# Performance work log

Measured on AMD Instinct MI355X. Metric: run time of the kernel, lower is better.

## Reference

```python
import jax, jax.numpy as jnp
import numpy as np
import math

B = 64        # graphs per batch
NPG = 2048    # nodes per graph
DEG = 4       # avg degree
EPG = NPG * DEG
N = B * NPG
E = B * EPG
F_IN = 4
H = 128
K1 = math.ceil(0.8 * NPG)   # 1639
K2 = math.ceil(0.8 * K1)    # 1312
K3 = math.ceil(0.8 * K2)    # 1050
ACT = 124


def setup_inputs() -> dict:
    key = jax.random.key(0)
    ks = jax.random.split(key, 20)
    x = jax.random.normal(ks[0], (N, F_IN), jnp.float32)
    off = (jnp.arange(B, dtype=jnp.int32) * NPG)[:, None]
    src = (jax.random.randint(ks[1], (B, EPG), 0, NPG, jnp.int32) + off).reshape(-1)
    dst = (jax.random.randint(ks[2], (B, EPG), 0, NPG, jnp.int32) + off).reshape(-1)

    def lin(k, fi, fo):
        return (jax.random.normal(k, (fi, fo), jnp.float32) / np.sqrt(fi)).astype(jnp.float32)

    return dict(
        x=x, src=src, dst=dst,
        W1=lin(ks[3], F_IN, H), b1=jnp.zeros((H,), jnp.float32),
        W2=lin(ks[4], H, H),    b2=jnp.zeros((H,), jnp.float32),
        W3=lin(ks[5], H, H),    b3=jnp.zeros((H,), jnp.float32),
        p1=jax.random.normal(ks[6], (H,), jnp.float32),
        p2=jax.random.normal(ks[7], (H,), jnp.float32),
        p3=jax.random.normal(ks[8], (H,), jnp.float32),
        lw1=lin(ks[9], 2 * H, H),  lb1=jnp.zeros((H,), jnp.float32),
        lw2=lin(ks[10], H, 64),    lb2=jnp.zeros((64,), jnp.float32),
        lw3=lin(ks[11], 64, ACT),  lb3=jnp.zeros((ACT,), jnp.float32),
    )


def gcn(x, W, b, src, dst, emask, n_nodes):
    # PyG GCNConv: add self loops, sym-norm deg^-1/2 A deg^-1/2, then bias
    h = x @ W                                  # [n, H]
    w = emask.astype(x.dtype)                  # [E]
    deg = jax.ops.segment_sum(w, dst, num_segments=n_nodes) + 1.0  # +1 self loop
    dis = jax.lax.rsqrt(deg)
    coef = dis[src] * dis[dst] * w             # [E]
    out = jax.ops.segment_sum(h[src] * coef[:, None], dst, num_segments=n_nodes)
    out = out + h * (dis * dis)[:, None]       # self-loop contribution
    return out + b


def topk_pool(x, p, src, dst, emask, n_per_graph, k):
    # TopKPooling: score = tanh(x.p/||p||); keep top ceil(ratio*n) per graph;
    # x_out = x[perm] * score[perm]; drop edges not fully inside kept set.
    score = jnp.tanh((x @ p) / jnp.linalg.norm(p))       # [B*n]
    vals, idx = jax.lax.top_k(score.reshape(B, n_per_graph), k)  # [B,k]
    xg = x.reshape(B, n_per_graph, -1)
    x_new = (jnp.take_along_axis(xg, idx[:, :, None], axis=1) * vals[:, :, None])
    x_new = x_new.reshape(B * k, -1)
    flat_idx = (idx + (jnp.arange(B, dtype=jnp.int32) * n_per_graph)[:, None]).reshape(-1)
    new_pos = jnp.full((B * n_per_graph,), -1, jnp.int32)
    new_pos = new_pos.at[flat_idx].set(jnp.arange(B * k, dtype=jnp.int32))
    ns, nd = new_pos[src], new_pos[dst]
    valid = emask & (ns >= 0) & (nd >= 0)
    ns = jnp.where(valid, ns, 0)
    nd = jnp.where(valid, nd, 0)
    return x_new, ns, nd, valid


def readout(x, k):
    # global_max_pool || global_mean_pool (uniform graph sizes)
    xr = x.reshape(B, k, -1)
    return jnp.concatenate([xr.max(axis=1), xr.mean(axis=1)], axis=1)  # [B, 2H]


def reference(x, src, dst, W1, b1, W2, b2, W3, b3, p1, p2, p3,
              lw1, lb1, lw2, lb2, lw3, lb3):
    emask = jnp.ones((E,), bool)
    h = jax.nn.relu(gcn(x, W1, b1, src, dst, emask, N))
    h, s1, d1, m1 = topk_pool(h, p1, src, dst, emask, NPG, K1)
    x1 = readout(h, K1)
    h = jax.nn.relu(gcn(h, W2, b2, s1, d1, m1, B * K1))
    h, s2, d2, m2 = topk_pool(h, p2, s1, d1, m1, K1, K2)
    x2 = readout(h, K2)
    h = jax.nn.relu(gcn(h, W3, b3, s2, d2, m2, B * K2))
    h, s3, d3, m3 = topk_pool(h, p3, s2, d2, m2, K2, K3)
    x3 = readout(h, K3)
    z = x1 + x2 + x3                                # [B, 256]
    z = jax.nn.relu(z @ lw1 + lb1)
    z = jax.nn.relu(z @ lw2 + lb2)
    # F.dropout(p=0.5) is identity in eval mode
    out = jax.nn.sigmoid(z @ lw3 + lb3)             # [B, 124]; squeeze(1) is no-op
    return out
```

## Files before the change

kernel.cpp:

```cpp
#include <hip/hip_runtime.h>
#include <math.h>

namespace {
constexpr int B_   = 64;
constexpr int NPG  = 2048;
constexpr int N0   = B_ * NPG;
constexpr int E0   = N0 * 4;
constexpr int H_   = 128;
constexpr int K1   = 1639, K2 = 1312, K3 = 1050;
constexpr int N1   = B_ * K1;
constexpr int N2   = B_ * K2;
constexpr int N3   = B_ * K3;
constexpr int ACT  = 124;
constexpr int RS   = 32;
}

__global__ __launch_bounds__(256) void mmh_k(const float* __restrict__ Xin,
                                             const int* __restrict__ selOld,
                                             const float* __restrict__ score,
                                             const float* __restrict__ W,
                                             float* __restrict__ C, int M)
{
    __shared__ float sA[64 * 128];
    int tid = threadIdx.x;
    int row0 = blockIdx.x * 64;
    #pragma unroll
    for (int ch = 0; ch < 8; ++ch) {
        int i = ch * 1024 + tid * 4;
        int r = i >> 7, c = i & 127;
        int g = selOld[row0 + r];
        float sc = score[g];
        float4 v = *(const float4*)(Xin + (size_t)g * H_ + c);
        v.x *= sc; v.y *= sc; v.z *= sc; v.w *= sc;
        *(float4*)(sA + i) = v;
    }
    __syncthreads();
    int c4 = (tid & 31) * 4;
    int rg = tid >> 5;
    const float* sArow = sA + rg * 8 * 128;
    float4 acc[8];
    #pragma unroll
    for (int q = 0; q < 8; ++q) acc[q] = make_float4(0.f, 0.f, 0.f, 0.f);

    const float* Wp = W + c4;
    float4 w0 = *(const float4*)(Wp + 0 * 128);
    float4 w1 = *(const float4*)(Wp + 1 * 128);
    float4 w2 = *(const float4*)(Wp + 2 * 128);
    float4 w3 = *(const float4*)(Wp + 3 * 128);
    #pragma unroll 1
    for (int g4 = 0; g4 < 31; ++g4) {
        int kk = g4 * 4;
        const float* Wn = Wp + (kk + 4) * 128;
        float4 n0 = *(const float4*)(Wn + 0 * 128);
        float4 n1 = *(const float4*)(Wn + 1 * 128);
        float4 n2 = *(const float4*)(Wn + 2 * 128);
        float4 n3 = *(const float4*)(Wn + 3 * 128);
        #pragma unroll
        for (int q = 0; q < 8; ++q) {
            float4 a = *(const float4*)(sArow + q * 128 + kk);
            acc[q].x += a.x * w0.x; acc[q].y += a.x * w0.y; acc[q].z += a.x * w0.z; acc[q].w += a.x * w0.w;
            acc[q].x += a.y * w1.x; acc[q].y += a.y * w1.y; acc[q].z += a.y * w1.z; acc[q].w += a.y * w1.w;
            acc[q].x += a.z * w2.x; acc[q].y += a.z * w2.y; acc[q].z += a.z * w2.z; acc[q].w += a.z * w2.w;
            acc[q].x += a.w * w3.x; acc[q].y += a.w * w3.y; acc[q].z += a.w * w3.z; acc[q].w += a.w * w3.w;
        }
        w0 = n0; w1 = n1; w2 = n2; w3 = n3;
    }
    {
        const int kk = 124;
        #pragma unroll
        for (int q = 0; q < 8; ++q) {
            float4 a = *(const float4*)(sArow + q * 128 + kk);
            acc[q].x += a.x * w0.x; acc[q].y += a.x * w0.y; acc[q].z += a.x * w0.z; acc[q].w += a.x * w0.w;
            acc[q].x += a.y * w1.x; acc[q].y += a.y * w1.y; acc[q].z += a.y * w1.z; acc[q].w += a.y * w1.w;
            acc[q].x += a.z * w2.x; acc[q].y += a.z * w2.y; acc[q].z += a.z * w2.z; acc[q].w += a.z * w2.w;
            acc[q].x += a.w * w3.x; acc[q].y += a.w * w3.y; acc[q].z += a.w * w3.z; acc[q].w += a.w * w3.w;
        }
    }
    #pragma unroll
    for (int q = 0; q < 8; ++q) {
        int r = row0 + rg * 8 + q;
        *(float4*)(C + (size_t)r * H_ + c4) = acc[q];
    }
}

__global__ void count_deg_k(const int* __restrict__ dst, int E, int* __restrict__ deg)
{
    int e = blockIdx.x * blockDim.x + threadIdx.x;
    if (e < E) atomicAdd(deg + dst[e], 1);
}

__global__ __launch_bounds__(1024) void scan1_k(const int* __restrict__ in, int* __restrict__ out,
                                                int* __restrict__ bsum, int n)
{
    __shared__ int s[1024];
    int t = threadIdx.x;
    int i = blockIdx.x * 1024 + t;
    int v = (i < n) ? in[i] : 0;
    s[t] = v;
    __syncthreads();
    for (int d = 1; d < 1024; d <<= 1) {
        int add = (t >= d) ? s[t - d] : 0;
        __syncthreads();
        s[t] += add;
        __syncthreads();
    }
    if (i < n) out[i] = s[t] - v;
    if (t == 1023) bsum[blockIdx.x] = s[1023];
}

__global__ __launch_bounds__(256) void scan2_k(int* __restrict__ bsum, int nb,
                                               int* __restrict__ totalOut,
                                               const float* __restrict__ p,
                                               float* __restrict__ invnOut)
{
    __shared__ int s[256];
    __shared__ float ps[128];
    int t = threadIdx.x;
    int v = (t < nb) ? bsum[t] : 0;
    s[t] = v;
    if (p && t < 128) ps[t] = p[t] * p[t];
    __syncthreads();
    for (int d = 1; d < 256; d <<= 1) {
        int add = (t >= d) ? s[t - d] : 0;
        __syncthreads();
        s[t] += add;
        __syncthreads();
    }
    if (t < nb) bsum[t] = s[t] - v;
    if (t == 0 && totalOut) *totalOut = s[255];
    for (int d = 64; d > 0; d >>= 1) {
        if (p && t < d) ps[t] += ps[t + d];
        __syncthreads();
    }
    if (p && t == 0) *invnOut = rsqrtf(ps[0]);
}

__global__ void scan3_k(int* __restrict__ out, const int* __restrict__ bsum, int n,
                        const int* __restrict__ deg, float* __restrict__ dis)
{
    int i = blockIdx.x * blockDim.x + threadIdx.x;
    if (i < n) {
        out[i] += bsum[i >> 10];
        dis[i] = rsqrtf((float)deg[i] + 1.0f);
    }
}

__global__ void fill_k(const int* __restrict__ src, const int* __restrict__ dst, int E,
                       const int* __restrict__ rowoff, int* __restrict__ cur,
                       int* __restrict__ esrc)
{
    int e = blockIdx.x * blockDim.x + threadIdx.x;
    if (e >= E) return;
    int d = dst[e];
    int pos = rowoff[d] + atomicAdd(cur + d, 1);
    esrc[pos] = src[e];
}

__global__ void remap_count_k(const int* __restrict__ osrc, const int* __restrict__ odst,
                              const int* __restrict__ ecntIn, int fixedE,
                              const int* __restrict__ newpos, int* __restrict__ deg)
{
    int E = ecntIn ? *ecntIn : fixedE;
    int e = blockIdx.x * blockDim.x + threadIdx.x;
    if (e >= E) return;
    int ns = newpos[osrc[e]];
    int nd = newpos[odst[e]];
    if (ns >= 0 && nd >= 0) atomicAdd(deg + nd, 1);
}

__global__ void remap_fill_k(const int* __restrict__ osrc, const int* __restrict__ odst,
                             const int* __restrict__ ecntIn, int fixedE,
                             const int* __restrict__ newpos, const int* __restrict__ rowoff,
                             int* __restrict__ cur,
                             int* __restrict__ esrc, int* __restrict__ edst)
{
    int E = ecntIn ? *ecntIn : fixedE;
    int e = blockIdx.x * blockDim.x + threadIdx.x;
    if (e >= E) return;
    int ns = newpos[osrc[e]];
    int nd = newpos[odst[e]];
    if (ns >= 0 && nd >= 0) {
        int pos = rowoff[nd] + atomicAdd(cur + nd, 1);
        esrc[pos] = ns;
        edst[pos] = nd;
    }
}

__global__ __launch_bounds__(256) void aggx_k(const float* __restrict__ X,
                                              const int* __restrict__ rowoff,
                                              const int* __restrict__ esrc,
                                              const float* __restrict__ dis,
                                              const float* __restrict__ W1,
                                              const float* __restrict__ b1,
                                              const float* __restrict__ p1,
                                              const float* __restrict__ invn,
                                              float* __restrict__ out,
                                              float* __restrict__ score,
                                              int npg, int Gb)
{
    __shared__ float sW[512];
    __shared__ float sb[128];
    __shared__ float sp[128];
    __shared__ float sxa[256 * 4];
    __shared__ float sdt[256];
    int tid = threadIdx.x;
    for (int i = tid; i < 512; i += 256) sW[i] = W1[i];
    if (tid < 128) { sb[tid] = b1[tid]; sp[tid] = p1[tid]; }
    int pb = blockIdx.x;
    int x8 = pb & 7;
    int m  = pb >> 3;
    int g  = x8 + 8 * (m / Gb);
    int lb = m % Gb;
    int nbase = g * npg + lb * 256;
    int n = nbase + tid;
    float dn = dis[n];
    float4 xa = *(const float4*)(X + (size_t)n * 4);
    float s2 = dn * dn;
    xa.x *= s2; xa.y *= s2; xa.z *= s2; xa.w *= s2;
    int beg = rowoff[n], end = rowoff[n + 1];
    for (int e = beg; e < end; ++e) {
        int s = esrc[e];
        float c = dis[s] * dn;
        float4 xs = *(const float4*)(X + (size_t)s * 4);
        xa.x += xs.x * c; xa.y += xs.y * c; xa.z += xs.z * c; xa.w += xs.w * c;
    }
    *(float4*)(sxa + tid * 4) = xa;
    __syncthreads();
    int wv = tid >> 6;
    int lane = tid & 63;
    int c0 = lane * 2;
    float wa0 = sW[c0],     wb0 = sW[128 + c0],     wc0 = sW[256 + c0],     wd0 = sW[384 + c0];
    float wa1 = sW[c0 + 1], wb1 = sW[128 + c0 + 1], wc1 = sW[256 + c0 + 1], wd1 = sW[384 + c0 + 1];
    float bb0 = sb[c0], bb1 = sb[c0 + 1];
    float pp0 = sp[c0], pp1 = sp[c0 + 1];
    #pragma unroll 4
    for (int ii = 0; ii < 64; ++ii) {
        int i = wv * 64 + ii;
        float4 a = *(const float4*)(sxa + i * 4);
        float o0 = fmaxf(a.x * wa0 + a.y * wb0 + a.z * wc0 + a.w * wd0 + bb0, 0.f);
        float o1 = fmaxf(a.x * wa1 + a.y * wb1 + a.z * wc1 + a.w * wd1 + bb1, 0.f);
        ((float2*)(out + (size_t)(nbase + i) * H_))[lane] = make_float2(o0, o1);
        float dt = o0 * pp0 + o1 * pp1;
        for (int mm = 32; mm > 0; mm >>= 1) dt += __shfl_xor(dt, mm);
        if (lane == 0) sdt[i] = dt;
    }
    __syncthreads();
    score[nbase + tid] = tanhf(sdt[tid] * invn[0]);
}

__global__ __launch_bounds__(256) void agg_k(const float* __restrict__ Hf,
                                             const int* __restrict__ rowoff,
                                             const int* __restrict__ esrc,
                                             const float* __restrict__ dis,
                                             const float* __restrict__ bias,
                                             const float* __restrict__ p,
                                             const float* __restrict__ invn,
                                             float* __restrict__ out,
                                             float* __restrict__ score,
                                             int npg, int Gb)
{
    int pb = blockIdx.x;
    int x8 = pb & 7;
    int m  = pb >> 3;
    int g  = x8 + 8 * (m / Gb);
    int lb = m % Gb;
    int j  = lb * 4 + (threadIdx.x >> 6);
    if (j >= npg) return;
    int n = g * npg + j;
    int lane = threadIdx.x & 63;
    int half = lane >> 5;
    int l4 = (lane & 31) * 4;
    float dn = dis[n];
    int beg = rowoff[n], end = rowoff[n + 1];
    float4 acc = make_float4(0.f, 0.f, 0.f, 0.f);
    for (int e = beg + half; e < end; e += 2) {
        int s = esrc[e];
        float c = dis[s] * dn;
        float4 v = *(const float4*)(Hf + (size_t)s * H_ + l4);
        acc.x += v.x * c; acc.y += v.y * c; acc.z += v.z * c; acc.w += v.w * c;
    }
    acc.x += __shfl_xor(acc.x, 32);
    acc.y += __shfl_xor(acc.y, 32);
    acc.z += __shfl_xor(acc.z, 32);
    acc.w += __shfl_xor(acc.w, 32);
    if (half == 0) {
        float4 hv = *(const float4*)(Hf + (size_t)n * H_ + l4);
        float4 bv = *(const float4*)(bias + l4);
        float s2 = dn * dn;
        float o0 = fmaxf(acc.x + hv.x * s2 + bv.x, 0.f);
        float o1 = fmaxf(acc.y + hv.y * s2 + bv.y, 0.f);
        float o2 = fmaxf(acc.z + hv.z * s2 + bv.z, 0.f);
        float o3 = fmaxf(acc.w + hv.w * s2 + bv.w, 0.f);
        *(float4*)(out + (size_t)n * H_ + l4) = make_float4(o0, o1, o2, o3);
        float4 pv = *(const float4*)(p + l4);
        float dt = o0 * pv.x + o1 * pv.y + o2 * pv.z + o3 * pv.w;
        for (int mm = 16; mm > 0; mm >>= 1) dt += __shfl_xor(dt, mm);
        if ((lane & 31) == 0) score[n] = tanhf(dt * invn[0]);
    }
}

__global__ __launch_bounds__(1024) void radix_topk_k(const float* __restrict__ score,
                                                     int n, int k,
                                                     int* __restrict__ selOld,
                                                     int* __restrict__ newpos)
{
    __shared__ unsigned long long key[2048];
    __shared__ int hist[256];
    __shared__ int sufs[256];
    __shared__ unsigned long long sh_prefix;
    __shared__ int sh_r, sh_done, sh_v, sh_rbin;
    __shared__ int cnt;
    int b = blockIdx.x;
    int t = threadIdx.x;
    const float* s = score + (size_t)b * n;
    #pragma unroll
    for (int h = 0; h < 2; ++h) {
        int i = t + h * 1024;
        unsigned long long pk = 0ull;
        if (i < n) {
            unsigned u = __float_as_uint(s[i]);
            u = (u & 0x80000000u) ? ~u : (u | 0x80000000u);
            pk = ((unsigned long long)u << 32) | (unsigned)(65535 - i);
        }
        key[i] = pk;
    }
    if (t == 0) { sh_prefix = 0ull; sh_r = k; sh_done = 0; cnt = 0; }
    __syncthreads();

    for (int lvl = 0; lvl < 8; ++lvl) {
        if (sh_done) break;
        int bs = 56 - 8 * lvl;
        if (t < 256) hist[t] = 0;
        __syncthreads();
        unsigned long long pref = sh_prefix;
        #pragma unroll
        for (int h = 0; h < 2; ++h) {
            int i = t + h * 1024;
            unsigned long long kk = key[i];
            if (kk != 0ull) {
                bool match = (lvl == 0) || ((kk >> (bs + 8)) == (pref >> (bs + 8)));
                if (match) atomicAdd(&hist[(int)((kk >> bs) & 255)], 1);
            }
        }
        __syncthreads();
        if (t < 256) sufs[t] = hist[t];
        __syncthreads();
        for (int d = 1; d < 256; d <<= 1) {
            int add = (t < 256 && t + d < 256) ? sufs[t + d] : 0;
            __syncthreads();
            if (t < 256) sufs[t] += add;
            __syncthreads();
        }
        if (t < 256) {
            int above = (t == 255) ? 0 : sufs[t + 1];
            if (sufs[t] >= sh_r && above < sh_r) {
                sh_v = t;
                sh_rbin = sh_r - above;
            }
        }
        __syncthreads();
        if (t == 0) {
            int v = sh_v;
            sh_prefix |= ((unsigned long long)v) << bs;
            sh_r = sh_rbin;
            if (hist[v] == sh_rbin) sh_done = 1;
        }
        __syncthreads();
    }
    unsigned long long thr = sh_prefix;
    #pragma unroll
    for (int h = 0; h < 2; ++h) {
        int i = t + h * 1024;
        if (i < n && key[i] >= thr) {
            int pos = atomicAdd(&cnt, 1);
            int oldg = b * n + i;
            selOld[b * k + pos] = oldg;
            newpos[oldg] = b * k + pos;
        }
    }
}

__global__ __launch_bounds__(512) void readout_part_k(const float* __restrict__ X,
                                                      const int* __restrict__ selOld,
                                                      const float* __restrict__ score,
                                                      int kRows, float* __restrict__ part)
{
    __shared__ float smax[16][128];
    __shared__ float ssum[16][128];
    int b = blockIdx.x / RS;
    int s = blockIdx.x % RS;
    int chunk = (kRows + RS - 1) / RS;
    int j0 = s * chunk;
    int j1 = min(kRows, j0 + chunk);
    int tid = threadIdx.x;
    int f4 = (tid & 31) * 4;
    int q = tid >> 5;
    float4 mx = make_float4(-3.4e38f, -3.4e38f, -3.4e38f, -3.4e38f);
    float4 sm = make_float4(0.f, 0.f, 0.f, 0.f);
    for (int j = j0 + q; j < j1; j += 16) {
        int g = selOld[b * kRows + j];
        float sc = score[g];
        float4 v = *(const float4*)(X + (size_t)g * H_ + f4);
        v.x *= sc; v.y *= sc; v.z *= sc; v.w *= sc;
        mx.x = fmaxf(mx.x, v.x); mx.y = fmaxf(mx.y, v.y);
        mx.z = fmaxf(mx.z, v.z); mx.w = fmaxf(mx.w, v.w);
        sm.x += v.x; sm.y += v.y; sm.z += v.z; sm.w += v.w;
    }
    *(float4*)&smax[q][f4] = mx;
    *(float4*)&ssum[q][f4] = sm;
    __syncthreads();
    if (tid < 128) {
        float m = smax[0][tid], a = ssum[0][tid];
        #pragma unroll
        for (int gq = 1; gq < 16; ++gq) {
            m = fmaxf(m, smax[gq][tid]);
            a += ssum[gq][tid];
        }
        float* pr = part + ((size_t)b * RS + s) * 256;
        pr[tid] = m;
        pr[128 + tid] = a;
    }
}

__global__ __launch_bounds__(256) void head_k(const float* __restrict__ part1,
                                              const float* __restrict__ part2,
                                              const float* __restrict__ part3,
                                              const float* __restrict__ lw1, const float* __restrict__ lb1,
                                              const float* __restrict__ lw2, const float* __restrict__ lb2,
                                              const float* __restrict__ lw3, const float* __restrict__ lb3,
                                              float* __restrict__ out)
{
    __shared__ float sZ[256];
    __shared__ float sZ1[128];
    __shared__ float sZ2[64];
    __shared__ float red[256];
    int b = blockIdx.x;
    int t = threadIdx.x;
    {
        int f = t & 127;
        const float* pr1 = part1 + (size_t)b * RS * 256;
        const float* pr2 = part2 + (size_t)b * RS * 256;
        const float* pr3 = part3 + (size_t)b * RS * 256;
        float zv;
        if (t < 128) {
            float m1 = -3.4e38f, m2 = -3.4e38f, m3 = -3.4e38f;
            #pragma unroll
            for (int s = 0; s < RS; ++s) {
                m1 = fmaxf(m1, pr1[s * 256 + f]);
                m2 = fmaxf(m2, pr2[s * 256 + f]);
                m3 = fmaxf(m3, pr3[s * 256 + f]);
            }
            zv = m1 + m2 + m3;
        } else {
            float s1 = 0.f, s2 = 0.f, s3 = 0.f;
            #pragma unroll
            for (int s = 0; s < RS; ++s) {
                s1 += pr1[s * 256 + 128 + f];
                s2 += pr2[s * 256 + 128 + f];
                s3 += pr3[s * 256 + 128 + f];
            }
            zv = s1 * (1.0f / (float)K1) + s2 * (1.0f / (float)K2) + s3 * (1.0f / (float)K3);
        }
        sZ[t] = zv;
    }
    __syncthreads();
    {
        int c = t & 127, h = t >> 7;
        float acc = 0.f;
        #pragma unroll
        for (int i = 0; i < 128; ++i) {
            int ii = h * 128 + i;
            acc += sZ[ii] * lw1[ii * 128 + c];
        }
        red[t] = acc;
        __syncthreads();
        if (t < 128) sZ1[t] = fmaxf(red[t] + red[128 + t] + lb1[t], 0.f);
        __syncthreads();
    }
    {
        int c = t & 63, q = t >> 6;
        float acc = 0.f;
        #pragma unroll
        for (int i = 0; i < 32; ++i) {
            int ii = q * 32 + i;
            acc += sZ1[ii] * lw2[ii * 64 + c];
        }
        red[t] = acc;
        __syncthreads();
        if (t < 64) sZ2[t] = fmaxf(red[t] + red[64 + t] + red[128 + t] + red[192 + t] + lb2[t], 0.f);
        __syncthreads();
    }
    {
        if (t < 2 * ACT) {
            int c = t >> 1, h = t & 1;
            float acc = 0.f;
            #pragma unroll
            for (int i = 0; i < 32; ++i) {
                int ii = h * 32 + i;
                acc += sZ2[ii] * lw3[ii * ACT + c];
            }
            red[t] = acc;
        }
        __syncthreads();
        if (t < ACT) {
            float s = red[2 * t] + red[2 * t + 1] + lb3[t];
            out[b * ACT + t] = 1.f / (1.f + expf(-s));
        }
    }
}

extern "C" void kernel_launch(void* const* d_in, const int* in_sizes, int n_in,
                              void* d_out, int out_size, void* d_ws, size_t ws_size,
                              hipStream_t stream)
{
    const float* x   = (const float*)d_in[0];
    const int*   src = (const int*)d_in[1];
    const int*   dst = (const int*)d_in[2];
    const float* W1  = (const float*)d_in[3];
    const float* b1  = (const float*)d_in[4];
    const float* W2  = (const float*)d_in[5];
    const float* b2  = (const float*)d_in[6];
    const float* W3  = (const float*)d_in[7];
    const float* b3  = (const float*)d_in[8];
    const float* p1  = (const float*)d_in[9];
    const float* p2  = (const float*)d_in[10];
    const float* p3  = (const float*)d_in[11];
    const float* lw1 = (const float*)d_in[12];
    const float* lb1 = (const float*)d_in[13];
    const float* lw2 = (const float*)d_in[14];
    const float* lb2 = (const float*)d_in[15];
    const float* lw3 = (const float*)d_in[16];
    const float* lb3 = (const float*)d_in[17];

    char* w = (char*)d_ws;
    size_t off = 0;
    auto alloc = [&](size_t bytes) -> void* {
        void* p = w + off;
        off = (off + bytes + 255) & ~(size_t)255;
        return p;
    };
    float* fA     = (float*)alloc((size_t)N0 * H_ * 4);
    float* fB     = (float*)alloc((size_t)N0 * H_ * 4);
    float* score  = (float*)alloc((size_t)N0 * 4);
    int*   newpos = (int*)  alloc((size_t)N0 * 4);
    int*   deg    = (int*)  alloc((size_t)(N0 + 1) * 4);
    int*   cur    = (int*)  alloc((size_t)N0 * 4);
    float* dis    = (float*)alloc((size_t)(N0 + 1) * 4);
    int*   selOld = (int*)  alloc((size_t)N1 * 4);
    int*   rowoff = (int*)  alloc((size_t)(N0 + 1) * 4);
    int*   bsum   = (int*)  alloc((size_t)1024 * 4);
    int*   cs0    = (int*)  alloc((size_t)E0 * 4);
    int*   cs1    = (int*)  alloc((size_t)E0 * 4);
    int*   cd1    = (int*)  alloc((size_t)E0 * 4);
    int*   cs2    = (int*)  alloc((size_t)E0 * 4);
    int*   cd2    = (int*)  alloc((size_t)E0 * 4);
    float* part1  = (float*)alloc((size_t)B_ * RS * 256 * 4);
    float* part2  = (float*)alloc((size_t)B_ * RS * 256 * 4);
    float* part3  = (float*)alloc((size_t)B_ * RS * 256 * 4);
    int*   ecnt   = (int*)  alloc(256);
    float* invn   = (float*)alloc(256);

    const size_t degcur_bytes = (size_t)((char*)cur - (char*)deg) + (size_t)N0 * 4;

    auto scan_rowoff = [&](int nNodes, int* totalOut, const float* p) {
        int n = nNodes + 1;
        int nb = (n + 1023) / 1024;
        scan1_k<<<nb, 1024, 0, stream>>>(deg, rowoff, bsum, n);
        scan2_k<<<1, 256, 0, stream>>>(bsum, nb, totalOut, p, invn);
        scan3_k<<<(n + 255) / 256, 256, 0, stream>>>(rowoff, bsum, n, deg, dis);
    };

    const int GbX = NPG / 256;
    const int Gb1 = (K1 + 3) / 4;
    const int Gb2 = (K2 + 3) / 4;

    hipMemsetAsync(deg, 0, degcur_bytes, stream);
    count_deg_k<<<E0 / 256, 256, 0, stream>>>(dst, E0, deg);
    scan_rowoff(N0, nullptr, p1);
    fill_k<<<E0 / 256, 256, 0, stream>>>(src, dst, E0, rowoff, cur, cs0);
    aggx_k<<<B_ * GbX, 256, 0, stream>>>(x, rowoff, cs0, dis, W1, b1, p1, invn, fB, score, NPG, GbX);

    hipMemsetAsync(newpos, 0xFF, (size_t)N0 * 4, stream);
    radix_topk_k<<<B_, 1024, 0, stream>>>(score, NPG, K1, selOld, newpos);
    readout_part_k<<<B_ * RS, 512, 0, stream>>>(fB, selOld, score, K1, part1);

    hipMemsetAsync(deg, 0, degcur_bytes, stream);
    remap_count_k<<<E0 / 256, 256, 0, stream>>>(src, dst, nullptr, E0, newpos, deg);
    scan_rowoff(N1, ecnt, p2);
    remap_fill_k<<<E0 / 256, 256, 0, stream>>>(src, dst, nullptr, E0, newpos, rowoff, cur, cs1, cd1);

    mmh_k<<<N1 / 64, 256, 0, stream>>>(fB, selOld, score, W2, fA, N1);
    agg_k<<<B_ * Gb1, 256, 0, stream>>>(fA, rowoff, cs1, dis, b2, p2, invn, fB, score, K1, Gb1);

    hipMemsetAsync(newpos, 0xFF, (size_t)N1 * 4, stream);
    radix_topk_k<<<B_, 1024, 0, stream>>>(score, K1, K2, selOld, newpos);
    readout_part_k<<<B_ * RS, 512, 0, stream>>>(fB, selOld, score, K2, part2);

    hipMemsetAsync(deg, 0, degcur_bytes, stream);
    remap_count_k<<<E0 / 256, 256, 0, stream>>>(cs1, cd1, ecnt, 0, newpos, deg);
    scan_rowoff(N2, nullptr, p3);
    remap_fill_k<<<E0 / 256, 256, 0, stream>>>(cs1, cd1, ecnt, 0, newpos, rowoff, cur, cs2, cd2);

    mmh_k<<<N2 / 64, 256, 0, stream>>>(fB, selOld, score, W3, fA, N2);
    agg_k<<<B_ * Gb2, 256, 0, stream>>>(fA, rowoff, cs2, dis, b3, p3, invn, fB, score, K2, Gb2);

    radix_topk_k<<<B_, 1024, 0, stream>>>(score, K2, K3, selOld, newpos);
    readout_part_k<<<B_ * RS, 512, 0, stream>>>(fB, selOld, score, K3, part3);

    head_k<<<B_, 256, 0, stream>>>(part1, part2, part3, lw1, lb1, lw2, lb2, lw3, lb3, (float*)d_out);
}
```

Before: 389.2 us.

## Use bf16 MFMA for hidden GCN linear layers with pre-packed transposed weights

Replaces the FP32 FMA inner loop of the hidden-layer matmul with bf16 MFMA 16x16x32 instructions. Activations are converted to bf16 into an XOR-swizzled shared tile, and weights are transposed and packed to bf16 by a small kernel on each call. This aims to cut the compute cost of the two 128x128 projections. In exchange it lowers precision to bf16 inputs, adds two tiny pack kernels, and writes the output as scalar stores instead of float4.

```diff
diff --git a/kernel.cpp b/kernel.cpp
--- a/kernel.cpp
+++ b/kernel.cpp
@@ -15,13 +15,31 @@
 constexpr int RS   = 32;
 }
 
+typedef short bf16x8 __attribute__((ext_vector_type(8)));
+typedef float f32x4  __attribute__((ext_vector_type(4)));
+
+__device__ __forceinline__ unsigned short f2bf(float f)
+{
+    unsigned x = __float_as_uint(f);
+    x = x + 0x7FFFu + ((x >> 16) & 1u);
+    return (unsigned short)(x >> 16);
+}
+
+__global__ void pack_k(const float* __restrict__ W, unsigned short* __restrict__ WT)
+{
+    int t = blockIdx.x * 256 + threadIdx.x;
+    int n = t >> 7, k = t & 127;
+    WT[n * 128 + k] = f2bf(W[k * 128 + n]);
+}
+
 __global__ __launch_bounds__(256) void mmh_k(const float* __restrict__ Xin,
                                              const int* __restrict__ selOld,
                                              const float* __restrict__ score,
-                                             const float* __restrict__ W,
+                                             const unsigned short* __restrict__ WT,
                                              float* __restrict__ C, int M)
 {
-    __shared__ float sA[64 * 128];
+    __shared__ unsigned short sA[64 * 128];
+    char* sAb = (char*)sA;
     int tid = threadIdx.x;
     int row0 = blockIdx.x * 64;
     #pragma unroll
@@ -31,55 +49,46 @@
         int g = selOld[row0 + r];
         float sc = score[g];
         float4 v = *(const float4*)(Xin + (size_t)g * H_ + c);
-        v.x *= sc; v.y *= sc; v.z *= sc; v.w *= sc;
-        *(float4*)(sA + i) = v;
-    }
-    __syncthreads();
-    int c4 = (tid & 31) * 4;
-    int rg = tid >> 5;
-    const float* sArow = sA + rg * 8 * 128;
-    float4 acc[8];
+        unsigned short h0 = f2bf(v.x * sc), h1 = f2bf(v.y * sc);
+        unsigned short h2 = f2bf(v.z * sc), h3 = f2bf(v.w * sc);
+        unsigned int lo = (unsigned int)h0 | ((unsigned int)h1 << 16);
+        unsigned int hi = (unsigned int)h2 | ((unsigned int)h3 << 16);
+        int off = (r * 256 + c * 2) ^ ((r & 7) << 4);
+        *(unsigned int*)(sAb + off)     = lo;
+        *(unsigned int*)(sAb + off + 4) = hi;
+    }
+    __syncthreads();
+
+    int w    = tid >> 6;
+    int lane = tid & 63;
+    int l16  = lane & 15;
+    int lq   = lane >> 4;
+    int arow = w * 16 + l16;
+    int abase = (arow * 256) ^ ((arow & 7) << 4);
+
+    f32x4 acc[8];
     #pragma unroll
-    for (int q = 0; q < 8; ++q) acc[q] = make_float4(0.f, 0.f, 0.f, 0.f);
-
-    const float* Wp = W + c4;
-    float4 w0 = *(const float4*)(Wp + 0 * 128);
-    float4 w1 = *(const float4*)(Wp + 1 * 128);
-    float4 w2 = *(const float4*)(Wp + 2 * 128);
-    float4 w3 = *(const float4*)(Wp + 3 * 128);
-    #pragma unroll 1
-    for (int g4 = 0; g4 < 31; ++g4) {
-        int kk = g4 * 4;
-        const float* Wn = Wp + (kk + 4) * 128;
-        float4 n0 = *(const float4*)(Wn + 0 * 128);
-        float4 n1 = *(const float4*)(Wn + 1 * 128);
-        float4 n2 = *(const float4*)(Wn + 2 * 128);
-        float4 n3 = *(const float4*)(Wn + 3 * 128);
+    for (int ct = 0; ct < 8; ++ct) acc[ct] = (f32x4){0.f, 0.f, 0.f, 0.f};
+
+    #pragma unroll
+    for (int ks = 0; ks < 4; ++ks) {
+        int aoff = (arow * 256 + ks * 64 + lq * 16) ^ ((arow & 7) << 4);
+        bf16x8 af = *(const bf16x8*)(sAb + aoff);
         #pragma unroll
-        for (int q = 0; q < 8; ++q) {
-            float4 a = *(const float4*)(sArow + q * 128 + kk);
-            acc[q].x += a.x * w0.x; acc[q].y += a.x * w0.y; acc[q].z += a.x * w0.z; acc[q].w += a.x * w0.w;
-            acc[q].x += a.y * w1.x; acc[q].y += a.y * w1.y; acc[q].z += a.y * w1.z; acc[q].w += a.y * w1.w;
-            acc[q].x += a.z * w2.x; acc[q].y += a.z * w2.y; acc[q].z += a.z * w2.z; acc[q].w += a.z * w2.w;
-            acc[q].x += a.w * w3.x; acc[q].y += a.w * w3.y; acc[q].z += a.w * w3.z; acc[q].w += a.w * w3.w;
-        }
-        w0 = n0; w1 = n1; w2 = n2; w3 = n3;
-    }
-    {
-        const int kk = 124;
-        #pragma unroll
-        for (int q = 0; q < 8; ++q) {
-            float4 a = *(const float4*)(sArow + q * 128 + kk);
-            acc[q].x += a.x * w0.x; acc[q].y += a.x * w0.y; acc[q].z += a.x * w0.z; acc[q].w += a.x * w0.w;
-            acc[q].x += a.y * w1.x; acc[q].y += a.y * w1.y; acc[q].z += a.y * w1.z; acc[q].w += a.y * w1.w;
-            acc[q].x += a.z * w2.x; acc[q].y += a.z * w2.y; acc[q].z += a.z * w2.z; acc[q].w += a.z * w2.w;
-            acc[q].x += a.w * w3.x; acc[q].y += a.w * w3.y; acc[q].z += a.w * w3.z; acc[q].w += a.w * w3.w;
+        for (int ct = 0; ct < 8; ++ct) {
+            const unsigned short* bp = WT + (ct * 16 + l16) * 128 + ks * 32 + lq * 8;
+            bf16x8 bf = *(const bf16x8*)bp;
+            acc[ct] = __builtin_amdgcn_mfma_f32_16x16x32_bf16(af, bf, acc[ct], 0, 0, 0);
         }
     }
     #pragma unroll
-    for (int q = 0; q < 8; ++q) {
-        int r = row0 + rg * 8 + q;
-        *(float4*)(C + (size_t)r * H_ + c4) = acc[q];
+    for (int ct = 0; ct < 8; ++ct) {
+        int col = ct * 16 + l16;
+        int rb  = row0 + w * 16 + lq * 4;
+        C[(size_t)(rb + 0) * H_ + col] = acc[ct][0];
+        C[(size_t)(rb + 1) * H_ + col] = acc[ct][1];
+        C[(size_t)(rb + 2) * H_ + col] = acc[ct][2];
+        C[(size_t)(rb + 3) * H_ + col] = acc[ct][3];
     }
 }
 
@@ -557,6 +566,8 @@
     float* part1  = (float*)alloc((size_t)B_ * RS * 256 * 4);
     float* part2  = (float*)alloc((size_t)B_ * RS * 256 * 4);
     float* part3  = (float*)alloc((size_t)B_ * RS * 256 * 4);
+    unsigned short* WT2 = (unsigned short*)alloc((size_t)128 * 128 * 2);
+    unsigned short* WT3 = (unsigned short*)alloc((size_t)128 * 128 * 2);
     int*   ecnt   = (int*)  alloc(256);
     float* invn   = (float*)alloc(256);
 
@@ -574,6 +585,9 @@
     const int Gb1 = (K1 + 3) / 4;
     const int Gb2 = (K2 + 3) / 4;
 
+    pack_k<<<64, 256, 0, stream>>>(W2, WT2);
+    pack_k<<<64, 256, 0, stream>>>(W3, WT3);
+
     hipMemsetAsync(deg, 0, degcur_bytes, stream);
     count_deg_k<<<E0 / 256, 256, 0, stream>>>(dst, E0, deg);
     scan_rowoff(N0, nullptr, p1);
@@ -589,7 +603,7 @@
     scan_rowoff(N1, ecnt, p2);
     remap_fill_k<<<E0 / 256, 256, 0, stream>>>(src, dst, nullptr, E0, newpos, rowoff, cur, cs1, cd1);
 
-    mmh_k<<<N1 / 64, 256, 0, stream>>>(fB, selOld, score, W2, fA, N1);
+    mmh_k<<<N1 / 64, 256, 0, stream>>>(fB, selOld, score, WT2, fA, N1);
     agg_k<<<B_ * Gb1, 256, 0, stream>>>(fA, rowoff, cs1, dis, b2, p2, invn, fB, score, K1, Gb1);
 
     hipMemsetAsync(newpos, 0xFF, (size_t)N1 * 4, stream);
@@ -601,7 +615,7 @@
     scan_rowoff(N2, nullptr, p3);
     remap_fill_k<<<E0 / 256, 256, 0, stream>>>(cs1, cd1, ecnt, 0, newpos, rowoff, cur, cs2, cd2);
 
-    mmh_k<<<N2 / 64, 256, 0, stream>>>(fB, selOld, score, W3, fA, N2);
+    mmh_k<<<N2 / 64, 256, 0, stream>>>(fB, selOld, score, WT3, fA, N2);
     agg_k<<<B_ * Gb2, 256, 0, stream>>>(fA, rowoff, cs2, dis, b3, p3, invn, fB, score, K2, Gb2);
 
     radix_topk_k<<<B_, 1024, 0, stream>>>(score, K2, K3, selOld, newpos);
```

Measured after the change: 362.7 us. -6.8%, faster.
